# Kernel tuning notes

Hardware: AMD Instinct MI355X
Metric: run time of the kernel (lower is better)

## Reference

```python
import jax, jax.numpy as jnp
import numpy as np

H = 4096          # hidden_size
I = 14336         # intermediate_size
SC = int(0.3 * I) # beta * I -> size of cached x_topk (4300)
HC = int(0.05 * I)# gamma * I -> helper top-k count (716)


def setup_inputs() -> dict:
    key = jax.random.key(0)
    ks = jax.random.split(key, 7)
    s = 0.02
    return {
        "x": jax.random.normal(ks[0], (1, 1, H), dtype=jnp.float32),
        "x_topk": jax.random.randint(ks[1], (SC,), 0, I, dtype=jnp.int64),
        "gate_w": jax.random.normal(ks[2], (I, H), dtype=jnp.float32) * s,
        "up_w": jax.random.normal(ks[3], (I, H), dtype=jnp.float32) * s,
        "down_w": jax.random.normal(ks[4], (H, I), dtype=jnp.float32) * s,
        "helper_w1": jax.random.normal(ks[5], (1024, H), dtype=jnp.float32) * s,
        "helper_w2": jax.random.normal(ks[6], (I, 1024), dtype=jnp.float32) * s,
    }


def reference(x, x_topk, gate_w, up_w, down_w, helper_w1, helper_w2):
    # --- sparsity predictor (SimpleLinearModel): two bias-free linears ---
    h = (x @ helper_w1.T) @ helper_w2.T                       # [1,1,I]
    up_mask_index = jax.lax.top_k(h.reshape(-1), HC)[1]       # [HC]

    # --- combine cached core indices with predicted indices, dedup ---
    combined = jnp.concatenate([x_topk.astype(jnp.int32),
                                up_mask_index.astype(jnp.int32)])  # [SC+HC]
    K = combined.shape[0]
    uniq = jnp.unique(combined, size=K, fill_value=I)         # padded with I
    valid = (uniq < I)                                        # [K] bool
    idx = jnp.where(valid, uniq, 0)                           # safe gather idx

    # --- gather weight rows/columns, reduced gated-MLP matmul ---
    gate_f = gate_w[idx]                                      # [K,H]
    up_f = up_w[idx]                                          # [K,H]
    gate_out = jnp.einsum('bsh,kh->bsk', x, gate_f)           # [1,1,K]
    up_out = jnp.einsum('bsh,kh->bsk', x, up_f)               # [1,1,K]
    tv = jax.nn.silu(gate_out) * up_out                       # act_fn = SiLU
    tv = tv * valid.astype(tv.dtype)                          # zero padded dups

    down_f = down_w[:, idx]                                   # [H,K]
    down_value = jnp.einsum('bsk,hk->bsh', tv, down_f)        # [1,1,H]
    return down_value
```

## Files before the change

kernel.cpp:

```cpp
#include <hip/hip_runtime.h>
#include <math.h>

#define H_DIM 4096
#define I_DIM 14336
#define HB_DIM 1024
#define SC_K 4300
#define HC_K 716

__device__ __forceinline__ unsigned sortable(float f) {
    unsigned u = __float_as_uint(f);
    return (u & 0x80000000u) ? ~u : (u | 0x80000000u);
}

__device__ __forceinline__ void compute_tv_row(const float* __restrict__ x,
                                               const float* __restrict__ gate_w,
                                               const float* __restrict__ up_w,
                                               float* __restrict__ tv, int row, int lane) {
    const float* gr = gate_w + (size_t)row * H_DIM;
    const float* ur = up_w + (size_t)row * H_DIM;
    float gs = 0.f, us = 0.f;
#pragma unroll 4
    for (int c = 0; c < H_DIM; c += 256) {
        int cc = c + lane * 4;
        float4 xv = *(const float4*)(x + cc);
        float4 g = *(const float4*)(gr + cc);
        float4 u = *(const float4*)(ur + cc);
        gs += g.x * xv.x + g.y * xv.y + g.z * xv.z + g.w * xv.w;
        us += u.x * xv.x + u.y * xv.y + u.z * xv.z + u.w * xv.w;
    }
#pragma unroll
    for (int o = 32; o >= 1; o >>= 1) {
        gs += __shfl_xor(gs, o);
        us += __shfl_xor(us, o);
    }
    if (lane == 0) {
        float s = gs / (1.f + expf(-gs));
        tv[row] = s * us;
    }
}

__global__ __launch_bounds__(256) void k1_h1_gateup(
    const float* __restrict__ x, const float* __restrict__ hw1,
    const int* __restrict__ x_topk, const float* __restrict__ gate_w,
    const float* __restrict__ up_w, float* __restrict__ h1,
    float* __restrict__ tv, int* __restrict__ claim) {
    int wid = threadIdx.x >> 6, lane = threadIdx.x & 63;
    int b = blockIdx.x;
    if (b < 256) {
        int row = b * 4 + wid;
        const float* mr = hw1 + (size_t)row * H_DIM;
        float s = 0.f;
#pragma unroll 4
        for (int c = 0; c < H_DIM; c += 256) {
            int cc = c + lane * 4;
            float4 m = *(const float4*)(mr + cc);
            float4 v = *(const float4*)(x + cc);
            s += m.x * v.x + m.y * v.y + m.z * v.z + m.w * v.w;
        }
#pragma unroll
        for (int o = 32; o >= 1; o >>= 1) s += __shfl_xor(s, o);
        if (lane == 0) h1[row] = s;
    } else {
        int gw = (b - 256) * 4 + wid;
        if (gw < SC_K) {
            int idx = x_topk[gw];
            int won = 0;
            if (lane == 0 && (unsigned)idx < (unsigned)I_DIM)
                won = (atomicExch(&claim[idx], 1) == 0);
            won = __shfl(won, 0);
            if (won) compute_tv_row(x, gate_w, up_w, tv, idx, lane);
        }
    }
}

__global__ __launch_bounds__(256) void k2_h(
    const float* __restrict__ h1, const float* __restrict__ hw2,
    float* __restrict__ hbuf) {
    int wid = threadIdx.x >> 6, lane = threadIdx.x & 63;
    int row = blockIdx.x * 4 + wid;
    const float* mr = hw2 + (size_t)row * HB_DIM;
    float s = 0.f;
#pragma unroll
    for (int c = 0; c < HB_DIM; c += 256) {
        int cc = c + lane * 4;
        float4 m = *(const float4*)(mr + cc);
        float4 v = *(const float4*)(h1 + cc);
        s += m.x * v.x + m.y * v.y + m.z * v.z + m.w * v.w;
    }
#pragma unroll
    for (int o = 32; o >= 1; o >>= 1) s += __shfl_xor(s, o);
    if (lane == 0) hbuf[row] = s;
}

__global__ __launch_bounds__(1024) void select_kernel(const float* __restrict__ h,
                                                      int* __restrict__ sel) {
    __shared__ unsigned bins[2048];
    __shared__ unsigned wpart[16];
    __shared__ int s_b, s_above;
    __shared__ int s_tie_cnt;
    __shared__ int tie_idx[2048];
    int tid = threadIdx.x;
    int lane = tid & 63, wid = tid >> 6;

    unsigned key[14];
#pragma unroll
    for (int j = 0; j < 14; ++j) key[j] = sortable(h[j * 1024 + tid]);

    if (tid == 0) s_tie_cnt = 0;

    int b1 = 0, b2 = 0;
    int above = 0;

    for (int pass = 0; pass < 3; ++pass) {
        int nb = (pass == 2) ? 1024 : 2048;
        bins[tid] = 0;
        if (nb == 2048) bins[tid + 1024] = 0;
        __syncthreads();
#pragma unroll
        for (int j = 0; j < 14; ++j) {
            unsigned u = key[j];
            bool in_sub = (pass == 0) ||
                          ((pass == 1) ? ((int)(u >> 21) == b1)
                                       : ((int)(u >> 21) == b1 && (int)((u >> 10) & 0x7FF) == b2));
            if (in_sub) {
                unsigned k = (pass == 0) ? (u >> 21)
                           : (pass == 1) ? ((u >> 10) & 0x7FF)
                                         : (u & 0x3FF);
                atomicAdd(&bins[k], 1u);
            }
        }
        __syncthreads();
        unsigned c0 = (2 * tid < nb) ? bins[2 * tid] : 0u;
        unsigned c1 = (2 * tid + 1 < nb) ? bins[2 * tid + 1] : 0u;
        unsigned s = c0 + c1;
        unsigned incl = s;
#pragma unroll
        for (int o = 1; o < 64; o <<= 1) {
            unsigned v = __shfl_up(incl, o);
            if (lane >= o) incl += v;
        }
        if (lane == 63) wpart[wid] = incl;
        __syncthreads();
        if (wid == 0 && lane < 16) {
            unsigned p = wpart[lane];
#pragma unroll
            for (int o = 1; o < 16; o <<= 1) {
                unsigned v = __shfl_up(p, o, 16);
                if (lane >= o) p += v;
            }
            wpart[lane] = p;
        }
        __syncthreads();
        unsigned total = wpart[15];
        unsigned base = (wid > 0 ? wpart[wid - 1] : 0u) + (incl - s);
        unsigned need = (unsigned)(HC_K - above);
        if (2 * tid < nb) {
            unsigned Pm1 = base, P = base + c0;
            if (total - P < need && total - Pm1 >= need) { s_b = 2 * tid; s_above = above + (int)(total - P); }
        }
        if (2 * tid + 1 < nb) {
            unsigned Pm1 = base + c0, P = base + c0 + c1;
            if (total - P < need && total - Pm1 >= need) { s_b = 2 * tid + 1; s_above = above + (int)(total - P); }
        }
        __syncthreads();
        if (pass == 0) b1 = s_b;
        else if (pass == 1) b2 = s_b;
        above = s_above;
        if (pass == 2) {
            unsigned T = ((unsigned)b1 << 21) | ((unsigned)b2 << 10) | (unsigned)s_b;
            int need2 = HC_K - above;
            __syncthreads();
#pragma unroll
            for (int j = 0; j < 14; ++j) {
                unsigned u = key[j];
                int i = j * 1024 + tid;
                if (u > T) sel[i] = 1;
                else if (u == T) {
                    int p = atomicAdd(&s_tie_cnt, 1);
                    if (p < 2048) tie_idx[p] = i;
                }
            }
            __syncthreads();
            int C = s_tie_cnt;
            if (C <= 2048) {
                for (int m = tid; m < C; m += 1024) {
                    int my = tie_idx[m];
                    int rank = 0;
                    for (int j = 0; j < C; ++j) rank += (tie_idx[j] < my) ? 1 : 0;
                    if (rank < need2) sel[my] = 1;
                }
            } else if (tid == 0) {
                int left = need2;
                for (int i = 0; i < I_DIM && left > 0; ++i)
                    if (sortable(h[i]) == T) { sel[i] = 1; --left; }
            }
        }
        __syncthreads();
    }
}

__global__ __launch_bounds__(256) void k3_gateup_rest(
    const float* __restrict__ x, const float* __restrict__ gate_w,
    const float* __restrict__ up_w, const int* __restrict__ sel,
    const int* __restrict__ claim, float* __restrict__ tv) {
    int wid = threadIdx.x >> 6, lane = threadIdx.x & 63;
    int row = blockIdx.x * 4 + wid;
    if (claim[row]) return;
    if (sel[row]) compute_tv_row(x, gate_w, up_w, tv, row, lane);
    else if (lane == 0) tv[row] = 0.f;
}

__global__ __launch_bounds__(256) void k4_down(
    const float* __restrict__ tv, const float* __restrict__ down_w,
    float* __restrict__ out) {
    int wid = threadIdx.x >> 6, lane = threadIdx.x & 63;
    int row = blockIdx.x * 4 + wid;
    const float* mr = down_w + (size_t)row * I_DIM;
    float s = 0.f;
#pragma unroll 4
    for (int c = 0; c < I_DIM; c += 256) {
        int cc = c + lane * 4;
        float4 m = *(const float4*)(mr + cc);
        float4 v = *(const float4*)(tv + cc);
        s += m.x * v.x + m.y * v.y + m.z * v.z + m.w * v.w;
    }
#pragma unroll
    for (int o = 32; o >= 1; o >>= 1) s += __shfl_xor(s, o);
    if (lane == 0) out[row] = s;
}

extern "C" void kernel_launch(void* const* d_in, const int* in_sizes, int n_in,
                              void* d_out, int out_size, void* d_ws, size_t ws_size,
                              hipStream_t stream) {
    const float* x      = (const float*)d_in[0];
    const int*   x_topk = (const int*)d_in[1];
    const float* gate_w = (const float*)d_in[2];
    const float* up_w   = (const float*)d_in[3];
    const float* down_w = (const float*)d_in[4];
    const float* hw1    = (const float*)d_in[5];
    const float* hw2    = (const float*)d_in[6];
    float* out = (float*)d_out;

    float* ws    = (float*)d_ws;
    float* h1    = ws;
    float* hbuf  = ws + 1024;
    float* tv    = ws + 1024 + I_DIM;
    int*   sel   = (int*)(ws + 1024 + 2 * I_DIM);
    int*   claim = sel + I_DIM;

    hipMemsetAsync(sel, 0, 2 * I_DIM * sizeof(int), stream);

    k1_h1_gateup<<<256 + (SC_K + 3) / 4, 256, 0, stream>>>(x, hw1, x_topk, gate_w,
                                                           up_w, h1, tv, claim);
    k2_h<<<I_DIM / 4, 256, 0, stream>>>(h1, hw2, hbuf);
    select_kernel<<<1, 1024, 0, stream>>>(hbuf, sel);
    k3_gateup_rest<<<I_DIM / 4, 256, 0, stream>>>(x, gate_w, up_w, sel, claim, tv);
    k4_down<<<H_DIM / 4, 256, 0, stream>>>(tv, down_w, out);
}
```

Baseline: 115.4 us.

## Compact residual selected rows into a list and drop claim/sel memset

The atomic claim dedup in k1 is removed, so duplicate x_topk rows are simply recomputed with identical writes. The select kernel now builds shared-memory bitmaps of cached and predicted indices and emits a compact list of predicted rows not already cached. It also zeroes tv for unselected rows. k3 launches only enough waves for that list instead of scanning all 14336 rows, and the memset launch is gone. In exchange, the single-block select kernel does more work and duplicate indices cost redundant row reads.

```diff
diff --git a/kernel.cpp b/kernel.cpp
--- a/kernel.cpp
+++ b/kernel.cpp
@@ -43,7 +43,7 @@
     const float* __restrict__ x, const float* __restrict__ hw1,
     const int* __restrict__ x_topk, const float* __restrict__ gate_w,
     const float* __restrict__ up_w, float* __restrict__ h1,
-    float* __restrict__ tv, int* __restrict__ claim) {
+    float* __restrict__ tv) {
     int wid = threadIdx.x >> 6, lane = threadIdx.x & 63;
     int b = blockIdx.x;
     if (b < 256) {
@@ -64,11 +64,8 @@
         int gw = (b - 256) * 4 + wid;
         if (gw < SC_K) {
             int idx = x_topk[gw];
-            int won = 0;
-            if (lane == 0 && (unsigned)idx < (unsigned)I_DIM)
-                won = (atomicExch(&claim[idx], 1) == 0);
-            won = __shfl(won, 0);
-            if (won) compute_tv_row(x, gate_w, up_w, tv, idx, lane);
+            if ((unsigned)idx < (unsigned)I_DIM)
+                compute_tv_row(x, gate_w, up_w, tv, idx, lane);
         }
     }
 }
@@ -92,12 +89,13 @@
     if (lane == 0) hbuf[row] = s;
 }
 
-__global__ __launch_bounds__(1024) void select_kernel(const float* __restrict__ h,
-                                                      int* __restrict__ sel) {
+__global__ __launch_bounds__(1024) void select_kernel(
+    const float* __restrict__ h, const int* __restrict__ x_topk,
+    float* __restrict__ tv, int* __restrict__ rlist, int* __restrict__ rcount) {
     __shared__ unsigned bins[2048];
     __shared__ unsigned wpart[16];
-    __shared__ int s_b, s_above;
-    __shared__ int s_tie_cnt;
+    __shared__ unsigned bitT[448], bitS[448];
+    __shared__ int s_b, s_above, s_tie_cnt, s_rc;
     __shared__ int tie_idx[2048];
     int tid = threadIdx.x;
     int lane = tid & 63, wid = tid >> 6;
@@ -106,10 +104,19 @@
 #pragma unroll
     for (int j = 0; j < 14; ++j) key[j] = sortable(h[j * 1024 + tid]);
 
-    if (tid == 0) s_tie_cnt = 0;
+    if (tid < 448) { bitT[tid] = 0; bitS[tid] = 0; }
+    if (tid == 0) { s_tie_cnt = 0; s_rc = 0; }
+    __syncthreads();
+
+    for (int k = tid; k < SC_K; k += 1024) {
+        int idx = x_topk[k];
+        if ((unsigned)idx < (unsigned)I_DIM) atomicOr(&bitT[idx >> 5], 1u << (idx & 31));
+    }
 
     int b1 = 0, b2 = 0;
     int above = 0;
+    unsigned T = 0;
+    int need2 = 0;
 
     for (int pass = 0; pass < 3; ++pass) {
         int nb = (pass == 2) ? 1024 : 2048;
@@ -167,47 +174,63 @@
         else if (pass == 1) b2 = s_b;
         above = s_above;
         if (pass == 2) {
-            unsigned T = ((unsigned)b1 << 21) | ((unsigned)b2 << 10) | (unsigned)s_b;
-            int need2 = HC_K - above;
-            __syncthreads();
-#pragma unroll
-            for (int j = 0; j < 14; ++j) {
-                unsigned u = key[j];
-                int i = j * 1024 + tid;
-                if (u > T) sel[i] = 1;
-                else if (u == T) {
-                    int p = atomicAdd(&s_tie_cnt, 1);
-                    if (p < 2048) tie_idx[p] = i;
-                }
+            T = ((unsigned)b1 << 21) | ((unsigned)b2 << 10) | (unsigned)s_b;
+            need2 = HC_K - above;
+        }
+        __syncthreads();
+    }
+
+#pragma unroll
+    for (int j = 0; j < 14; ++j) {
+        unsigned u = key[j];
+        int i = j * 1024 + tid;
+        if (u > T) atomicOr(&bitS[i >> 5], 1u << (i & 31));
+        else if (u == T) {
+            int p = atomicAdd(&s_tie_cnt, 1);
+            if (p < 2048) tie_idx[p] = i;
+        }
+    }
+    __syncthreads();
+    int C = s_tie_cnt;
+    if (C <= 2048) {
+        for (int m = tid; m < C; m += 1024) {
+            int my = tie_idx[m];
+            int rank = 0;
+            for (int j = 0; j < C; ++j) rank += (tie_idx[j] < my) ? 1 : 0;
+            if (rank < need2) atomicOr(&bitS[my >> 5], 1u << (my & 31));
+        }
+    } else if (tid == 0) {
+        int left = need2;
+        for (int i = 0; i < I_DIM && left > 0; ++i)
+            if (sortable(h[i]) == T) { atomicOr(&bitS[i >> 5], 1u << (i & 31)); --left; }
+    }
+    __syncthreads();
+
+#pragma unroll
+    for (int j = 0; j < 14; ++j) {
+        int i = j * 1024 + tid;
+        bool t = (bitT[i >> 5] >> (i & 31)) & 1u;
+        bool sl = (bitS[i >> 5] >> (i & 31)) & 1u;
+        if (!t) {
+            if (sl) {
+                int p = atomicAdd(&s_rc, 1);
+                rlist[p] = i;
+            } else {
+                tv[i] = 0.f;
             }
-            __syncthreads();
-            int C = s_tie_cnt;
-            if (C <= 2048) {
-                for (int m = tid; m < C; m += 1024) {
-                    int my = tie_idx[m];
-                    int rank = 0;
-                    for (int j = 0; j < C; ++j) rank += (tie_idx[j] < my) ? 1 : 0;
-                    if (rank < need2) sel[my] = 1;
-                }
-            } else if (tid == 0) {
-                int left = need2;
-                for (int i = 0; i < I_DIM && left > 0; ++i)
-                    if (sortable(h[i]) == T) { sel[i] = 1; --left; }
-            }
-        }
-        __syncthreads();
-    }
-}
-
-__global__ __launch_bounds__(256) void k3_gateup_rest(
+        }
+    }
+    __syncthreads();
+    if (tid == 0) *rcount = s_rc;
+}
+
+__global__ __launch_bounds__(256) void k3_residual(
     const float* __restrict__ x, const float* __restrict__ gate_w,
-    const float* __restrict__ up_w, const int* __restrict__ sel,
-    const int* __restrict__ claim, float* __restrict__ tv) {
-    int wid = threadIdx.x >> 6, lane = threadIdx.x & 63;
-    int row = blockIdx.x * 4 + wid;
-    if (claim[row]) return;
-    if (sel[row]) compute_tv_row(x, gate_w, up_w, tv, row, lane);
-    else if (lane == 0) tv[row] = 0.f;
+    const float* __restrict__ up_w, const int* __restrict__ rlist,
+    const int* __restrict__ rcount, float* __restrict__ tv) {
+    int wid = threadIdx.x >> 6, lane = threadIdx.x & 63;
+    int gw = blockIdx.x * 4 + wid;
+    if (gw < *rcount) compute_tv_row(x, gate_w, up_w, tv, rlist[gw], lane);
 }
 
 __global__ __launch_bounds__(256) void k4_down(
@@ -245,15 +268,13 @@
     float* h1    = ws;
     float* hbuf  = ws + 1024;
     float* tv    = ws + 1024 + I_DIM;
-    int*   sel   = (int*)(ws + 1024 + 2 * I_DIM);
-    int*   claim = sel + I_DIM;
-
-    hipMemsetAsync(sel, 0, 2 * I_DIM * sizeof(int), stream);
+    int*   rlist = (int*)(ws + 1024 + 2 * I_DIM);
+    int*   rcount = rlist + 768;
 
     k1_h1_gateup<<<256 + (SC_K + 3) / 4, 256, 0, stream>>>(x, hw1, x_topk, gate_w,
-                                                           up_w, h1, tv, claim);
+                                                           up_w, h1, tv);
     k2_h<<<I_DIM / 4, 256, 0, stream>>>(h1, hw2, hbuf);
-    select_kernel<<<1, 1024, 0, stream>>>(hbuf, sel);
-    k3_gateup_rest<<<I_DIM / 4, 256, 0, stream>>>(x, gate_w, up_w, sel, claim, tv);
+    select_kernel<<<1, 1024, 0, stream>>>(hbuf, x_topk, tv, rlist, rcount);
+    k3_residual<<<(HC_K + 3) / 4, 256, 0, stream>>>(x, gate_w, up_w, rlist, rcount, tv);
     k4_down<<<H_DIM / 4, 256, 0, stream>>>(tv, down_w, out);
 }
```

After: 103.7 us. 1.11x faster.
